# Kernel tuning notes

Hardware: AMD Instinct MI355X
Metric: run time of the kernel (lower is better)

## Reference

```python
import jax, jax.numpy as jnp
import numpy as np

O, I, B, G, BITS = 11008, 4096, 2048, 128, 3
N = I // G  # n_groups = 32
# Lloyd-Max optimal 8-level quantizer for unit Gaussian (3-bit PolarQuant codebook)
LLOYD_MAX_3BIT = [-2.1519, -1.3439, -0.7560, -0.2451, 0.2451, 0.7560, 1.3439, 2.1519]


def fwht(v):
    """Unnormalized fast Walsh-Hadamard transform along last axis (power-of-2 length)."""
    g = v.shape[-1]
    y = v.reshape(-1, g)
    h = 1
    while h < g:
        y = y.reshape(-1, g // (2 * h), 2, h)
        a, b = y[:, :, 0, :], y[:, :, 1, :]
        y = jnp.stack([a + b, a - b], axis=2).reshape(-1, g)
        h *= 2
    return y.reshape(v.shape)


def rotate(v, s1, s2):
    """Orthonormal randomized rotation R(v) = D2 * H * D1 * v / sqrt(G)."""
    g = v.shape[-1]
    return s2 * fwht(v * s1) * (1.0 / jnp.sqrt(jnp.asarray(g, v.dtype)))


def unpack3(packed):
    """Unpack 3-bit indices: [..., G//8*3] uint8 -> [..., G] int32 (matches unpack_indices)."""
    p = packed.reshape(*packed.shape[:-1], -1, 3).astype(jnp.int32)
    b0, b1, b2 = p[..., 0], p[..., 1], p[..., 2]
    outs = [
        b0 & 7, (b0 >> 3) & 7, ((b0 >> 6) | (b1 << 2)) & 7, (b1 >> 1) & 7,
        (b1 >> 4) & 7, ((b1 >> 7) | (b2 << 1)) & 7, (b2 >> 2) & 7, (b2 >> 5) & 7,
    ]
    return jnp.stack(outs, axis=-1).reshape(*packed.shape[:-1], -1)


def setup_inputs() -> dict:
    key = jax.random.key(0)
    kx, kw, k1, k2 = jax.random.split(key, 4)
    centroids = jnp.asarray(LLOYD_MAX_3BIT, dtype=jnp.float32)
    signs1 = jnp.where(jax.random.bernoulli(k1, 0.5, (G,)), 1.0, -1.0).astype(jnp.float32)
    signs2 = jnp.where(jax.random.bernoulli(k2, 0.5, (G,)), 1.0, -1.0).astype(jnp.float32)
    x = jax.random.normal(kx, (B, I), dtype=jnp.float32)
    # Quantize a dense weight exactly as TurboQuantWrapper.__init__ does.
    W = jax.random.normal(kw, (O, I), dtype=jnp.float32) * 0.02
    grouped = W.reshape(O, N, G)
    r = rotate(grouped, signs1, signs2)                     # [O,N,G] rotated groups
    gnorm = jnp.sqrt((r * r).sum(-1))                        # [O,N] (= ||w|| per group)
    dirn = r * jnp.sqrt(jnp.float32(G)) / (gnorm[..., None] + 1e-12)
    bnd = (centroids[:-1] + centroids[1:]) * 0.5
    idx = jnp.searchsorted(bnd, dirn)                        # nearest-centroid [O,N,G]
    q = centroids[idx]
    # norm correction: least-squares rescale of group norm against codebook hits
    norms = gnorm * (dirn * q).sum(-1) / ((q * q).sum(-1) + 1e-12)   # [O,N]
    # 3-bit packing: 8 indices -> 3 bytes (pack_indices, bits=3)
    v = np.asarray(idx, dtype=np.int32).reshape(O * N, G // 8, 8)
    b0 = v[..., 0] | (v[..., 1] << 3) | ((v[..., 2] & 3) << 6)
    b1 = (v[..., 2] >> 2) | (v[..., 3] << 1) | (v[..., 4] << 4) | ((v[..., 5] & 1) << 7)
    b2 = (v[..., 5] >> 1) | (v[..., 6] << 2) | (v[..., 7] << 5)
    packed = np.stack([b0, b1, b2], axis=-1).astype(np.uint8).reshape(O * N, G // 8 * 3)
    return {
        "x": x,
        "packed_weight": jnp.asarray(packed),
        "norms": norms.astype(jnp.float32),
        "centroids": centroids,
        "signs1": signs1,
        "signs2": signs2,
    }


def reference(x, packed_weight, norms, centroids, signs1, signs2):
    o, n = norms.shape
    g = signs1.shape[0]
    idx = unpack3(packed_weight.reshape(o, n, -1))           # [O,N,G] int32
    # FWHT-on-input: rotate each input group (fused kernel's input transform)
    rx = rotate(x.reshape(x.shape[0], n, g), signs1, signs2)  # [B,N,G]
    # Dequantized weight in rotated space: norm * centroid / sqrt(G)
    wq = centroids[idx] * (norms / jnp.sqrt(jnp.float32(g)))[:, :, None]  # [O,N,G]
    # x . w = R(x) . R(w) since R is orthonormal
    return jnp.einsum("bng,ong->bo", rx, wq)                 # [B,O]
```

## Files before the change

kernel.cpp:

```cpp
#include <hip/hip_runtime.h>

typedef unsigned int u32;
typedef unsigned short u16;

typedef short bf16x8 __attribute__((ext_vector_type(8)));
typedef float f32x4 __attribute__((ext_vector_type(4)));

#define GM 2048
#define GN 11008
#define GK 4096
#define NGRP 32
#define GSZ 128

#define CAST_G(p) ((const __attribute__((address_space(1))) void*)(p))
#define CAST_L(p) ((__attribute__((address_space(3))) void*)(p))
#define BAR() __builtin_amdgcn_s_barrier()
#define SCHED0() __builtin_amdgcn_sched_barrier(0)

__device__ __forceinline__ u16 f2bf(float f) {
    u32 u = __builtin_bit_cast(u32, f);
    u32 r = (u + 0x7FFFu + ((u >> 16) & 1u)) >> 16;
    return (u16)r;
}

__global__ __launch_bounds__(256) void rotate_kernel(
    const float* __restrict__ x, const float* __restrict__ s1,
    const float* __restrict__ s2, u32* __restrict__ rx) {
    int gid  = blockIdx.x * 256 + threadIdx.x;
    int grp  = gid >> 6;
    int lane = gid & 63;

    const float2* xp = (const float2*)(x + (size_t)grp * GSZ);
    float2 xv  = xp[lane];
    float2 s1v = ((const float2*)s1)[lane];
    float2 s2v = ((const float2*)s2)[lane];

    float e0 = xv.x * s1v.x;
    float e1 = xv.y * s1v.y;
    {
        float a = e0 + e1, b = e0 - e1;
        e0 = a; e1 = b;
    }
    #pragma unroll
    for (int hb = 1; hb <= 32; hb <<= 1) {
        float t0 = __shfl_xor(e0, hb, 64);
        float t1 = __shfl_xor(e1, hb, 64);
        bool up = (lane & hb) != 0;
        e0 = up ? (t0 - e0) : (e0 + t0);
        e1 = up ? (t1 - e1) : (e1 + t1);
    }
    const float inv = 0.08838834764831845f;
    u32 lo = f2bf(e0 * s2v.x * inv);
    u32 hi = f2bf(e1 * s2v.y * inv);
    rx[gid] = lo | (hi << 16);
}

__device__ __forceinline__ float cent3(int i) {
    int m3 = (i >= 4) ? (i - 4) : (3 - i);
    float mag = (m3 >= 2) ? ((m3 == 3) ? 2.1519f : 1.3439f)
                          : ((m3 == 1) ? 0.756f  : 0.2451f);
    return (i >= 4) ? mag : -mag;
}

__global__ __launch_bounds__(256) void dequant_kernel(
    const u32* __restrict__ p32, const float* __restrict__ norms,
    u16* __restrict__ wq) {
    int u = blockIdx.x * 256 + threadIdx.x;
    int g_idx = u >> 2;

    float scale = norms[g_idx] * 0.08838834764831845f;

    u32 w0 = p32[(size_t)u * 3 + 0];
    u32 w1 = p32[(size_t)u * 3 + 1];
    u32 w2 = p32[(size_t)u * 3 + 2];

    u32 tri[4];
    if (((w0 | w1 | w2) & 0xFFFFFF00u) == 0u) {
        const u32* pi = p32 + (size_t)u * 12;
        u32 b[12];
        #pragma unroll
        for (int k = 0; k < 12; ++k) b[k] = pi[k];
        #pragma unroll
        for (int t = 0; t < 4; ++t)
            tri[t] = b[3*t] | (b[3*t+1] << 8) | (b[3*t+2] << 16);
    } else {
        tri[0] = w0 & 0xFFFFFFu;
        tri[1] = (w0 >> 24) | ((w1 & 0xFFFFu) << 8);
        tri[2] = (w1 >> 16) | ((w2 & 0xFFu) << 16);
        tri[3] = w2 >> 8;
    }

    u32 ow[16];
    #pragma unroll
    for (int t = 0; t < 4; ++t) {
        u32 v = tri[t];
        #pragma unroll
        for (int k = 0; k < 4; ++k) {
            int i0 = (int)((v >> (6*k))     & 7u);
            int i1 = (int)((v >> (6*k + 3)) & 7u);
            u32 lo = f2bf(cent3(i0) * scale);
            u32 hi = f2bf(cent3(i1) * scale);
            ow[t*4 + k] = lo | (hi << 16);
        }
    }
    u32* op = (u32*)(wq + (size_t)u * 32);
    #pragma unroll
    for (int k = 0; k < 16; ++k) op[k] = ow[k];
}

__device__ __forceinline__ void stage_half(const u16* g, char* ldst, int rowOff, int tt) {
    __builtin_amdgcn_global_load_lds(CAST_G(g + (size_t)rowOff * GK + tt * 64),
                                     CAST_L(ldst), 16, 0, 0);
    __builtin_amdgcn_global_load_lds(CAST_G(g + (size_t)(rowOff + 64) * GK + tt * 64),
                                     CAST_L(ldst + 8192), 16, 0, 0);
}

template<int BUF>
__device__ __forceinline__ void ktile4(int t, char* lds,
                                       const u16* gA, const u16* gB,
                                       int sB, int aBase, int bBase, int sw0, int sw1,
                                       f32x4 (&acc)[8][4]) {
    const int AB  = BUF * 32768;
    const int BB  = 65536 + BUF * 32768;
    const int BBo = 65536 + (BUF ^ 1) * 32768;

    bf16x8 aF[4][2], b0F[2][2], b1F[2][2];
    bool s1 = (t < 63), s2 = (t < 62);

    #pragma unroll
    for (int mj = 0; mj < 4; ++mj) {
        aF[mj][0] = *(const bf16x8*)(lds + AB + aBase + mj * 4096 + sw0);
        aF[mj][1] = *(const bf16x8*)(lds + AB + aBase + mj * 4096 + sw1);
    }
    #pragma unroll
    for (int nj = 0; nj < 2; ++nj) {
        b0F[nj][0] = *(const bf16x8*)(lds + BB + bBase + nj * 8192 + sw0);
        b0F[nj][1] = *(const bf16x8*)(lds + BB + bBase + nj * 8192 + sw1);
    }
    if (s1) stage_half(gB, lds + BBo + 16384 + sB, 128, t + 1);
    BAR(); SCHED0();
    __builtin_amdgcn_s_setprio(1);
    #pragma unroll
    for (int mj = 0; mj < 4; ++mj)
        #pragma unroll
        for (int nj = 0; nj < 2; ++nj)
            #pragma unroll
            for (int kk = 0; kk < 2; ++kk)
                acc[mj][nj] = __builtin_amdgcn_mfma_f32_16x16x32_bf16(
                    aF[mj][kk], b0F[nj][kk], acc[mj][nj], 0, 0, 0);
    __builtin_amdgcn_s_setprio(0);
    BAR();

    #pragma unroll
    for (int nj = 0; nj < 2; ++nj) {
        b1F[nj][0] = *(const bf16x8*)(lds + BB + 16384 + bBase + nj * 8192 + sw0);
        b1F[nj][1] = *(const bf16x8*)(lds + BB + 16384 + bBase + nj * 8192 + sw1);
    }
    if (s2) stage_half(gA, lds + AB + sB, 0, t + 2);
    BAR(); SCHED0();
    __builtin_amdgcn_s_setprio(1);
    #pragma unroll
    for (int mj = 0; mj < 4; ++mj)
        #pragma unroll
        for (int nj = 0; nj < 2; ++nj)
            #pragma unroll
            for (int kk = 0; kk < 2; ++kk)
                acc[mj][2 + nj] = __builtin_amdgcn_mfma_f32_16x16x32_bf16(
                    aF[mj][kk], b1F[nj][kk], acc[mj][2 + nj], 0, 0, 0);
    __builtin_amdgcn_s_setprio(0);
    BAR();

    #pragma unroll
    for (int mj = 0; mj < 4; ++mj) {
        aF[mj][0] = *(const bf16x8*)(lds + AB + 16384 + aBase + mj * 4096 + sw0);
        aF[mj][1] = *(const bf16x8*)(lds + AB + 16384 + aBase + mj * 4096 + sw1);
    }
    if (s2) stage_half(gB, lds + BB + sB, 0, t + 2);
    BAR(); SCHED0();
    __builtin_amdgcn_s_setprio(1);
    #pragma unroll
    for (int mj = 0; mj < 4; ++mj)
        #pragma unroll
        for (int nj = 0; nj < 2; ++nj)
            #pragma unroll
            for (int kk = 0; kk < 2; ++kk)
                acc[4 + mj][nj] = __builtin_amdgcn_mfma_f32_16x16x32_bf16(
                    aF[mj][kk], b0F[nj][kk], acc[4 + mj][nj], 0, 0, 0);
    __builtin_amdgcn_s_setprio(0);
    BAR();

    if (s2) stage_half(gA, lds + AB + 16384 + sB, 128, t + 2);
    BAR(); SCHED0();
    __builtin_amdgcn_s_setprio(1);
    #pragma unroll
    for (int mj = 0; mj < 4; ++mj)
        #pragma unroll
        for (int nj = 0; nj < 2; ++nj)
            #pragma unroll
            for (int kk = 0; kk < 2; ++kk)
                acc[4 + mj][2 + nj] = __builtin_amdgcn_mfma_f32_16x16x32_bf16(
                    aF[mj][kk], b1F[nj][kk], acc[4 + mj][2 + nj], 0, 0, 0);
    __builtin_amdgcn_s_setprio(0);
    if (s2) { asm volatile("s_waitcnt vmcnt(6)" ::: "memory"); }
    else    { asm volatile("s_waitcnt vmcnt(0)" ::: "memory"); }
    BAR();
}

__device__ __forceinline__ void gemm_big(int tau, int tid, char* lds,
                                         const u16* A, const u16* Bw, float* C) {
    int lane = tid & 63;
    int wv   = tid >> 6;
    int wr   = wv >> 2;
    int wc   = wv & 3;

    int m0 = (tau & 7) * 256;
    int n0 = (tau >> 3) * 256;

    int srow = tid >> 3;
    int c16  = (tid & 7) ^ (srow & 7);
    const u16* gA = A  + (size_t)(m0 + srow) * GK + c16 * 8;
    const u16* gB = Bw + (size_t)(n0 + srow) * GK + c16 * 8;
    int sB = wv * 1024;

    int aBase = (wr * 16 + (lane & 15)) * 128;
    int bBase = (wc * 16 + (lane & 15)) * 128;
    int sw0 = (((lane >> 4))     ^ (lane & 7)) << 4;
    int sw1 = (((lane >> 4) + 4) ^ (lane & 7)) << 4;

    f32x4 acc[8][4] = {};

    stage_half(gA, lds + sB,                 0,   0);
    stage_half(gB, lds + 65536 + sB,         0,   0);
    stage_half(gA, lds + 16384 + sB,         128, 0);
    stage_half(gB, lds + 65536 + 16384 + sB, 128, 0);
    stage_half(gA, lds + 32768 + sB,         0,   1);
    stage_half(gB, lds + 65536 + 32768 + sB, 0,   1);
    stage_half(gA, lds + 32768 + 16384 + sB, 128, 1);
    asm volatile("s_waitcnt vmcnt(6)" ::: "memory");
    BAR();

    for (int tt = 0; tt < 64; tt += 2) {
        ktile4<0>(tt,     lds, gA, gB, sB, aBase, bBase, sw0, sw1, acc);
        ktile4<1>(tt + 1, lds, gA, gB, sB, aBase, bBase, sw0, sw1, acc);
    }

    int cr = (lane >> 4) * 4;
    int cc = lane & 15;
    #pragma unroll
    for (int mh = 0; mh < 2; ++mh)
        #pragma unroll
        for (int mj = 0; mj < 4; ++mj)
            #pragma unroll
            for (int nh = 0; nh < 2; ++nh)
                #pragma unroll
                for (int nj = 0; nj < 2; ++nj) {
                    float* cp = C + (size_t)(m0 + mh * 128 + wr * 16 + mj * 32 + cr) * GN
                                  + (n0 + nh * 128 + wc * 16 + nj * 64 + cc);
                    #pragma unroll
                    for (int j = 0; j < 4; ++j)
                        __builtin_nontemporal_store(acc[mh * 4 + mj][nh * 2 + nj][j],
                                                    cp + (size_t)j * GN);
                }
}

template<int BUF>
__device__ __forceinline__ void ktile2(int t, char* lds,
                                       const u16* gA, const u16* gB,
                                       int sB, int aBase, int bBase, int sw0, int sw1,
                                       f32x4 (&acc)[4][4]) {
    const int AB  = BUF * 16384;
    const int BB  = 49152 + BUF * 32768;
    const int NB  = (BUF + 2 >= 3) ? (BUF - 1) : (BUF + 2);
    const int ABn = NB * 16384;
    const int BBn = 49152 + NB * 32768;

    bf16x8 aF[4][2], bF[2][2];
    bool s2 = (t < 62);

    #pragma unroll
    for (int mj = 0; mj < 4; ++mj) {
        aF[mj][0] = *(const bf16x8*)(lds + AB + aBase + mj * 4096 + sw0);
        aF[mj][1] = *(const bf16x8*)(lds + AB + aBase + mj * 4096 + sw1);
    }
    #pragma unroll
    for (int nj = 0; nj < 2; ++nj) {
        bF[nj][0] = *(const bf16x8*)(lds + BB + bBase + nj * 8192 + sw0);
        bF[nj][1] = *(const bf16x8*)(lds + BB + bBase + nj * 8192 + sw1);
    }
    if (s2) {
        stage_half(gA, lds + ABn + sB, 0, t + 2);
        stage_half(gB, lds + BBn + sB, 0, t + 2);
    }
    BAR(); SCHED0();
    __builtin_amdgcn_s_setprio(1);
    #pragma unroll
    for (int mj = 0; mj < 4; ++mj)
        #pragma unroll
        for (int nj = 0; nj < 2; ++nj)
            #pragma unroll
            for (int kk = 0; kk < 2; ++kk)
                acc[mj][nj] = __builtin_amdgcn_mfma_f32_16x16x32_bf16(
                    aF[mj][kk], bF[nj][kk], acc[mj][nj], 0, 0, 0);
    __builtin_amdgcn_s_setprio(0);
    BAR();

    #pragma unroll
    for (int nj = 0; nj < 2; ++nj) {
        bF[nj][0] = *(const bf16x8*)(lds + BB + 16384 + bBase + nj * 8192 + sw0);
        bF[nj][1] = *(const bf16x8*)(lds + BB + 16384 + bBase + nj * 8192 + sw1);
    }
    if (s2) stage_half(gB, lds + BBn + 16384 + sB, 128, t + 2);
    BAR(); SCHED0();
    __builtin_amdgcn_s_setprio(1);
    #pragma unroll
    for (int mj = 0; mj < 4; ++mj)
        #pragma unroll
        for (int nj = 0; nj < 2; ++nj)
            #pragma unroll
            for (int kk = 0; kk < 2; ++kk)
                acc[mj][2 + nj] = __builtin_amdgcn_mfma_f32_16x16x32_bf16(
                    aF[mj][kk], bF[nj][kk], acc[mj][2 + nj], 0, 0, 0);
    __builtin_amdgcn_s_setprio(0);
    if (s2) { asm volatile("s_waitcnt vmcnt(6)" ::: "memory"); }
    else    { asm volatile("s_waitcnt vmcnt(0)" ::: "memory"); }
    BAR();
}

__device__ __forceinline__ void gemm_tail(int bid, int tid, char* lds,
                                          const u16* A, const u16* Bw, float* C) {
    int lane = tid & 63;
    int wv   = tid >> 6;
    int wr   = wv >> 2;
    int wc   = wv & 3;

    int swz = (bid & 7) * 22 + (bid >> 3);
    int nt  = swz >> 4;
    int mh  = swz & 15;
    int m0  = mh * 128;
    int n0  = 8192 + nt * 256;

    int srow = tid >> 3;
    int c16  = (tid & 7) ^ (srow & 7);
    const u16* gA = A  + (size_t)(m0 + srow) * GK + c16 * 8;
    const u16* gB = Bw + (size_t)(n0 + srow) * GK + c16 * 8;
    int sB = wv * 1024;

    int aBase = (wr * 16 + (lane & 15)) * 128;
    int bBase = (wc * 16 + (lane & 15)) * 128;
    int sw0 = (((lane >> 4))     ^ (lane & 7)) << 4;
    int sw1 = (((lane >> 4) + 4) ^ (lane & 7)) << 4;

    f32x4 acc[4][4] = {};

    stage_half(gA, lds + sB,                 0,   0);
    stage_half(gB, lds + 49152 + sB,         0,   0);
    stage_half(gB, lds + 49152 + 16384 + sB, 128, 0);
    stage_half(gA, lds + 16384 + sB,         0,   1);
    stage_half(gB, lds + 81920 + sB,         0,   1);
    stage_half(gB, lds + 81920 + 16384 + sB, 128, 1);
    asm volatile("s_waitcnt vmcnt(6)" ::: "memory");
    BAR();

    for (int tt = 0; tt < 63; tt += 3) {
        ktile2<0>(tt,     lds, gA, gB, sB, aBase, bBase, sw0, sw1, acc);
        ktile2<1>(tt + 1, lds, gA, gB, sB, aBase, bBase, sw0, sw1, acc);
        ktile2<2>(tt + 2, lds, gA, gB, sB, aBase, bBase, sw0, sw1, acc);
    }
    ktile2<0>(63, lds, gA, gB, sB, aBase, bBase, sw0, sw1, acc);

    int cr = (lane >> 4) * 4;
    int cc = lane & 15;
    #pragma unroll
    for (int mj = 0; mj < 4; ++mj)
        #pragma unroll
        for (int nj = 0; nj < 4; ++nj) {
            float* cp = C + (size_t)(m0 + wr * 16 + mj * 32 + cr) * GN
                          + (n0 + wc * 16 + nj * 64 + cc);
            #pragma unroll
            for (int j = 0; j < 4; ++j)
                __builtin_nontemporal_store(acc[mj][nj][j], cp + (size_t)j * GN);
        }
}

__global__ __launch_bounds__(512, 1) void gemm_all_kernel(
    const u16* __restrict__ A, const u16* __restrict__ Bw,
    float* __restrict__ C) {
    extern __shared__ char lds[];
    int bid = blockIdx.x;
    if (bid < 256) gemm_big (bid,       threadIdx.x, lds, A, Bw, C);
    else           gemm_tail(bid - 256, threadIdx.x, lds, A, Bw, C);
}

extern "C" void kernel_launch(void* const* d_in, const int* in_sizes, int n_in,
                              void* d_out, int out_size, void* d_ws, size_t ws_size,
                              hipStream_t stream) {
    const float* x      = (const float*)d_in[0];
    const void*  packed = d_in[1];
    const float* norms  = (const float*)d_in[2];
    const float* s1     = (const float*)d_in[4];
    const float* s2     = (const float*)d_in[5];
    float* out          = (float*)d_out;

    size_t rx_bytes = (size_t)GM * GK * 2;
    size_t wq_bytes = (size_t)GN * GK * 2;
    if (ws_size < rx_bytes + wq_bytes) return;

    u16* rx = (u16*)d_ws;
    u16* wq = rx + (size_t)GM * GK;

    rotate_kernel<<<dim3((GM * NGRP * 64) / 256), dim3(256), 0, stream>>>(
        x, s1, s2, (u32*)rx);

    dequant_kernel<<<dim3((GN * NGRP * 4) / 256), dim3(256), 0, stream>>>(
        (const u32*)packed, norms, wq);

    hipFuncSetAttribute((const void*)gemm_all_kernel,
                        hipFuncAttributeMaxDynamicSharedMemorySize, 147456);
    gemm_all_kernel<<<dim3(432), dim3(512), 147456, stream>>>(rx, wq, out);
}
```

Baseline: 219.5 us.

## Merge prep kernels and prefetch next k-tile fragments across tile boundary

```diff
diff --git a/kernel.cpp b/kernel.cpp
--- a/kernel.cpp
+++ b/kernel.cpp
@@ -23,38 +23,6 @@
     return (u16)r;
 }
 
-__global__ __launch_bounds__(256) void rotate_kernel(
-    const float* __restrict__ x, const float* __restrict__ s1,
-    const float* __restrict__ s2, u32* __restrict__ rx) {
-    int gid  = blockIdx.x * 256 + threadIdx.x;
-    int grp  = gid >> 6;
-    int lane = gid & 63;
-
-    const float2* xp = (const float2*)(x + (size_t)grp * GSZ);
-    float2 xv  = xp[lane];
-    float2 s1v = ((const float2*)s1)[lane];
-    float2 s2v = ((const float2*)s2)[lane];
-
-    float e0 = xv.x * s1v.x;
-    float e1 = xv.y * s1v.y;
-    {
-        float a = e0 + e1, b = e0 - e1;
-        e0 = a; e1 = b;
-    }
-    #pragma unroll
-    for (int hb = 1; hb <= 32; hb <<= 1) {
-        float t0 = __shfl_xor(e0, hb, 64);
-        float t1 = __shfl_xor(e1, hb, 64);
-        bool up = (lane & hb) != 0;
-        e0 = up ? (t0 - e0) : (e0 + t0);
-        e1 = up ? (t1 - e1) : (e1 + t1);
-    }
-    const float inv = 0.08838834764831845f;
-    u32 lo = f2bf(e0 * s2v.x * inv);
-    u32 hi = f2bf(e1 * s2v.y * inv);
-    rx[gid] = lo | (hi << 16);
-}
-
 __device__ __forceinline__ float cent3(int i) {
     int m3 = (i >= 4) ? (i - 4) : (3 - i);
     float mag = (m3 >= 2) ? ((m3 == 3) ? 2.1519f : 1.3439f)
@@ -62,50 +30,85 @@
     return (i >= 4) ? mag : -mag;
 }
 
-__global__ __launch_bounds__(256) void dequant_kernel(
+#define ROT_BLOCKS (GM * NGRP / 4)
+#define DQ_BLOCKS  (GN * NGRP * 4 / 256)
+
+__global__ __launch_bounds__(256) void prep_kernel(
+    const float* __restrict__ x, const float* __restrict__ s1,
+    const float* __restrict__ s2, u32* __restrict__ rx,
     const u32* __restrict__ p32, const float* __restrict__ norms,
     u16* __restrict__ wq) {
-    int u = blockIdx.x * 256 + threadIdx.x;
-    int g_idx = u >> 2;
-
-    float scale = norms[g_idx] * 0.08838834764831845f;
-
-    u32 w0 = p32[(size_t)u * 3 + 0];
-    u32 w1 = p32[(size_t)u * 3 + 1];
-    u32 w2 = p32[(size_t)u * 3 + 2];
-
-    u32 tri[4];
-    if (((w0 | w1 | w2) & 0xFFFFFF00u) == 0u) {
-        const u32* pi = p32 + (size_t)u * 12;
-        u32 b[12];
-        #pragma unroll
-        for (int k = 0; k < 12; ++k) b[k] = pi[k];
-        #pragma unroll
-        for (int t = 0; t < 4; ++t)
-            tri[t] = b[3*t] | (b[3*t+1] << 8) | (b[3*t+2] << 16);
+    if (blockIdx.x < ROT_BLOCKS) {
+        int gid  = blockIdx.x * 256 + threadIdx.x;
+        int grp  = gid >> 6;
+        int lane = gid & 63;
+
+        const float2* xp = (const float2*)(x + (size_t)grp * GSZ);
+        float2 xv  = xp[lane];
+        float2 s1v = ((const float2*)s1)[lane];
+        float2 s2v = ((const float2*)s2)[lane];
+
+        float e0 = xv.x * s1v.x;
+        float e1 = xv.y * s1v.y;
+        {
+            float a = e0 + e1, b = e0 - e1;
+            e0 = a; e1 = b;
+        }
+        #pragma unroll
+        for (int hb = 1; hb <= 32; hb <<= 1) {
+            float t0 = __shfl_xor(e0, hb, 64);
+            float t1 = __shfl_xor(e1, hb, 64);
+            bool up = (lane & hb) != 0;
+            e0 = up ? (t0 - e0) : (e0 + t0);
+            e1 = up ? (t1 - e1) : (e1 + t1);
+        }
+        const float inv = 0.08838834764831845f;
+        u32 lo = f2bf(e0 * s2v.x * inv);
+        u32 hi = f2bf(e1 * s2v.y * inv);
+        rx[gid] = lo | (hi << 16);
     } else {
-        tri[0] = w0 & 0xFFFFFFu;
-        tri[1] = (w0 >> 24) | ((w1 & 0xFFFFu) << 8);
-        tri[2] = (w1 >> 16) | ((w2 & 0xFFu) << 16);
-        tri[3] = w2 >> 8;
-    }
-
-    u32 ow[16];
-    #pragma unroll
-    for (int t = 0; t < 4; ++t) {
-        u32 v = tri[t];
-        #pragma unroll
-        for (int k = 0; k < 4; ++k) {
-            int i0 = (int)((v >> (6*k))     & 7u);
-            int i1 = (int)((v >> (6*k + 3)) & 7u);
-            u32 lo = f2bf(cent3(i0) * scale);
-            u32 hi = f2bf(cent3(i1) * scale);
-            ow[t*4 + k] = lo | (hi << 16);
-        }
-    }
-    u32* op = (u32*)(wq + (size_t)u * 32);
-    #pragma unroll
-    for (int k = 0; k < 16; ++k) op[k] = ow[k];
+        int u = (blockIdx.x - ROT_BLOCKS) * 256 + threadIdx.x;
+        int g_idx = u >> 2;
+
+        float scale = norms[g_idx] * 0.08838834764831845f;
+
+        u32 w0 = p32[(size_t)u * 3 + 0];
+        u32 w1 = p32[(size_t)u * 3 + 1];
+        u32 w2 = p32[(size_t)u * 3 + 2];
+
+        u32 tri[4];
+        if (((w0 | w1 | w2) & 0xFFFFFF00u) == 0u) {
+            const u32* pi = p32 + (size_t)u * 12;
+            u32 b[12];
+            #pragma unroll
+            for (int k = 0; k < 12; ++k) b[k] = pi[k];
+            #pragma unroll
+            for (int t = 0; t < 4; ++t)
+                tri[t] = b[3*t] | (b[3*t+1] << 8) | (b[3*t+2] << 16);
+        } else {
+            tri[0] = w0 & 0xFFFFFFu;
+            tri[1] = (w0 >> 24) | ((w1 & 0xFFFFu) << 8);
+            tri[2] = (w1 >> 16) | ((w2 & 0xFFu) << 16);
+            tri[3] = w2 >> 8;
+        }
+
+        u32 ow[16];
+        #pragma unroll
+        for (int t = 0; t < 4; ++t) {
+            u32 v = tri[t];
+            #pragma unroll
+            for (int k = 0; k < 4; ++k) {
+                int i0 = (int)((v >> (6*k))     & 7u);
+                int i1 = (int)((v >> (6*k + 3)) & 7u);
+                u32 lo = f2bf(cent3(i0) * scale);
+                u32 hi = f2bf(cent3(i1) * scale);
+                ow[t*4 + k] = lo | (hi << 16);
+            }
+        }
+        u32* op = (u32*)(wq + (size_t)u * 32);
+        #pragma unroll
+        for (int k = 0; k < 16; ++k) op[k] = ow[k];
+    }
 }
 
 __device__ __forceinline__ void stage_half(const u16* g, char* ldst, int rowOff, int tt) {
@@ -119,45 +122,42 @@
 __device__ __forceinline__ void ktile4(int t, char* lds,
                                        const u16* gA, const u16* gB,
                                        int sB, int aBase, int bBase, int sw0, int sw1,
+                                       bf16x8 (&aFx)[4][2], bf16x8 (&aFy)[4][2],
+                                       bf16x8 (&b0F)[2][2], bf16x8 (&b1F)[2][2],
                                        f32x4 (&acc)[8][4]) {
     const int AB  = BUF * 32768;
     const int BB  = 65536 + BUF * 32768;
+    const int ABo = (BUF ^ 1) * 32768;
     const int BBo = 65536 + (BUF ^ 1) * 32768;
 
-    bf16x8 aF[4][2], b0F[2][2], b1F[2][2];
     bool s1 = (t < 63), s2 = (t < 62);
-
-    #pragma unroll
-    for (int mj = 0; mj < 4; ++mj) {
-        aF[mj][0] = *(const bf16x8*)(lds + AB + aBase + mj * 4096 + sw0);
-        aF[mj][1] = *(const bf16x8*)(lds + AB + aBase + mj * 4096 + sw1);
-    }
-    #pragma unroll
-    for (int nj = 0; nj < 2; ++nj) {
-        b0F[nj][0] = *(const bf16x8*)(lds + BB + bBase + nj * 8192 + sw0);
-        b0F[nj][1] = *(const bf16x8*)(lds + BB + bBase + nj * 8192 + sw1);
-    }
-    if (s1) stage_half(gB, lds + BBo + 16384 + sB, 128, t + 1);
-    BAR(); SCHED0();
-    __builtin_amdgcn_s_setprio(1);
-    #pragma unroll
-    for (int mj = 0; mj < 4; ++mj)
-        #pragma unroll
-        for (int nj = 0; nj < 2; ++nj)
-            #pragma unroll
-            for (int kk = 0; kk < 2; ++kk)
-                acc[mj][nj] = __builtin_amdgcn_mfma_f32_16x16x32_bf16(
-                    aF[mj][kk], b0F[nj][kk], acc[mj][nj], 0, 0, 0);
-    __builtin_amdgcn_s_setprio(0);
-    BAR();
 
     #pragma unroll
     for (int nj = 0; nj < 2; ++nj) {
         b1F[nj][0] = *(const bf16x8*)(lds + BB + 16384 + bBase + nj * 8192 + sw0);
         b1F[nj][1] = *(const bf16x8*)(lds + BB + 16384 + bBase + nj * 8192 + sw1);
     }
+    if (s1) stage_half(gB, lds + BBo + 16384 + sB, 128, t + 1);
+    SCHED0(); BAR(); SCHED0();
+    __builtin_amdgcn_s_setprio(1);
+    #pragma unroll
+    for (int mj = 0; mj < 4; ++mj)
+        #pragma unroll
+        for (int nj = 0; nj < 2; ++nj)
+            #pragma unroll
+            for (int kk = 0; kk < 2; ++kk)
+                acc[mj][nj] = __builtin_amdgcn_mfma_f32_16x16x32_bf16(
+                    aFx[mj][kk], b0F[nj][kk], acc[mj][nj], 0, 0, 0);
+    __builtin_amdgcn_s_setprio(0);
+    BAR();
+
+    #pragma unroll
+    for (int mj = 0; mj < 4; ++mj) {
+        aFy[mj][0] = *(const bf16x8*)(lds + AB + 16384 + aBase + mj * 4096 + sw0);
+        aFy[mj][1] = *(const bf16x8*)(lds + AB + 16384 + aBase + mj * 4096 + sw1);
+    }
     if (s2) stage_half(gA, lds + AB + sB, 0, t + 2);
-    BAR(); SCHED0();
+    SCHED0(); BAR(); SCHED0();
     __builtin_amdgcn_s_setprio(1);
     #pragma unroll
     for (int mj = 0; mj < 4; ++mj)
@@ -166,17 +166,12 @@
             #pragma unroll
             for (int kk = 0; kk < 2; ++kk)
                 acc[mj][2 + nj] = __builtin_amdgcn_mfma_f32_16x16x32_bf16(
-                    aF[mj][kk], b1F[nj][kk], acc[mj][2 + nj], 0, 0, 0);
-    __builtin_amdgcn_s_setprio(0);
-    BAR();
-
-    #pragma unroll
-    for (int mj = 0; mj < 4; ++mj) {
-        aF[mj][0] = *(const bf16x8*)(lds + AB + 16384 + aBase + mj * 4096 + sw0);
-        aF[mj][1] = *(const bf16x8*)(lds + AB + 16384 + aBase + mj * 4096 + sw1);
-    }
+                    aFx[mj][kk], b1F[nj][kk], acc[mj][2 + nj], 0, 0, 0);
+    __builtin_amdgcn_s_setprio(0);
+    BAR();
+
     if (s2) stage_half(gB, lds + BB + sB, 0, t + 2);
-    BAR(); SCHED0();
+    SCHED0(); BAR(); SCHED0();
     __builtin_amdgcn_s_setprio(1);
     #pragma unroll
     for (int mj = 0; mj < 4; ++mj)
@@ -185,12 +180,27 @@
             #pragma unroll
             for (int kk = 0; kk < 2; ++kk)
                 acc[4 + mj][nj] = __builtin_amdgcn_mfma_f32_16x16x32_bf16(
-                    aF[mj][kk], b0F[nj][kk], acc[4 + mj][nj], 0, 0, 0);
-    __builtin_amdgcn_s_setprio(0);
-    BAR();
-
+                    aFy[mj][kk], b0F[nj][kk], acc[4 + mj][nj], 0, 0, 0);
+    __builtin_amdgcn_s_setprio(0);
+    if (s2) { asm volatile("s_waitcnt vmcnt(8)" ::: "memory"); }
+    else    { asm volatile("s_waitcnt vmcnt(0)" ::: "memory"); }
+    BAR();
+
+    if (s1) {
+        SCHED0();
+        #pragma unroll
+        for (int mj = 0; mj < 4; ++mj) {
+            aFx[mj][0] = *(const bf16x8*)(lds + ABo + aBase + mj * 4096 + sw0);
+            aFx[mj][1] = *(const bf16x8*)(lds + ABo + aBase + mj * 4096 + sw1);
+        }
+        #pragma unroll
+        for (int nj = 0; nj < 2; ++nj) {
+            b0F[nj][0] = *(const bf16x8*)(lds + BBo + bBase + nj * 8192 + sw0);
+            b0F[nj][1] = *(const bf16x8*)(lds + BBo + bBase + nj * 8192 + sw1);
+        }
+    }
     if (s2) stage_half(gA, lds + AB + 16384 + sB, 128, t + 2);
-    BAR(); SCHED0();
+    SCHED0(); BAR(); SCHED0();
     __builtin_amdgcn_s_setprio(1);
     #pragma unroll
     for (int mj = 0; mj < 4; ++mj)
@@ -199,7 +209,7 @@
             #pragma unroll
             for (int kk = 0; kk < 2; ++kk)
                 acc[4 + mj][2 + nj] = __builtin_amdgcn_mfma_f32_16x16x32_bf16(
-                    aF[mj][kk], b1F[nj][kk], acc[4 + mj][2 + nj], 0, 0, 0);
+                    aFy[mj][kk], b1F[nj][kk], acc[4 + mj][2 + nj], 0, 0, 0);
     __builtin_amdgcn_s_setprio(0);
     if (s2) { asm volatile("s_waitcnt vmcnt(6)" ::: "memory"); }
     else    { asm volatile("s_waitcnt vmcnt(0)" ::: "memory"); }
@@ -228,6 +238,7 @@
     int sw1 = (((lane >> 4) + 4) ^ (lane & 7)) << 4;
 
     f32x4 acc[8][4] = {};
+    bf16x8 aFx[4][2], aFy[4][2], b0F[2][2], b1F[2][2];
 
     stage_half(gA, lds + sB,                 0,   0);
     stage_half(gB, lds + 65536 + sB,         0,   0);
@@ -237,11 +248,23 @@
     stage_half(gB, lds + 65536 + 32768 + sB, 0,   1);
     stage_half(gA, lds + 32768 + 16384 + sB, 128, 1);
     asm volatile("s_waitcnt vmcnt(6)" ::: "memory");
-    BAR();
+    BAR(); SCHED0();
+    #pragma unroll
+    for (int mj = 0; mj < 4; ++mj) {
+        aFx[mj][0] = *(const bf16x8*)(lds + aBase + mj * 4096 + sw0);
+        aFx[mj][1] = *(const bf16x8*)(lds + aBase + mj * 4096 + sw1);
+    }
+    #pragma unroll
+    for (int nj = 0; nj < 2; ++nj) {
+        b0F[nj][0] = *(const bf16x8*)(lds + 65536 + bBase + nj * 8192 + sw0);
+        b0F[nj][1] = *(const bf16x8*)(lds + 65536 + bBase + nj * 8192 + sw1);
+    }
 
     for (int tt = 0; tt < 64; tt += 2) {
-        ktile4<0>(tt,     lds, gA, gB, sB, aBase, bBase, sw0, sw1, acc);
-        ktile4<1>(tt + 1, lds, gA, gB, sB, aBase, bBase, sw0, sw1, acc);
+        ktile4<0>(tt,     lds, gA, gB, sB, aBase, bBase, sw0, sw1,
+                  aFx, aFy, b0F, b1F, acc);
+        ktile4<1>(tt + 1, lds, gA, gB, sB, aBase, bBase, sw0, sw1,
+                  aFx, aFy, b0F, b1F, acc);
     }
 
     int cr = (lane >> 4) * 4;
@@ -408,11 +431,8 @@
     u16* rx = (u16*)d_ws;
     u16* wq = rx + (size_t)GM * GK;
 
-    rotate_kernel<<<dim3((GM * NGRP * 64) / 256), dim3(256), 0, stream>>>(
-        x, s1, s2, (u32*)rx);
-
-    dequant_kernel<<<dim3((GN * NGRP * 4) / 256), dim3(256), 0, stream>>>(
-        (const u32*)packed, norms, wq);
+    prep_kernel<<<dim3(ROT_BLOCKS + DQ_BLOCKS), dim3(256), 0, stream>>>(
+        x, s1, s2, (u32*)rx, (const u32*)packed, norms, wq);
 
     hipFuncSetAttribute((const void*)gemm_all_kernel,
                         hipFuncAttributeMaxDynamicSharedMemorySize, 147456);
```

New measurement: 221.6 us. Within noise of the previous version (+0.9%).
